# Performance work log

Hardware: AMD Instinct MI355X
Metric: run time of the kernel (lower is better)

Reference implementation:

```python
import jax, jax.numpy as jnp
import numpy as np

E = 32      # embed_dim
F = 64      # ff_dim
S = 256     # input_dim == seq_len (each feature is a token)
O = 8       # output_dim
B = 2048    # batch


def _layernorm(x, g, b, eps=1e-5):
    mu = jnp.mean(x, axis=-1, keepdims=True)
    var = jnp.mean((x - mu) ** 2, axis=-1, keepdims=True)
    return (x - mu) * jax.lax.rsqrt(var + eps) * g + b


def setup_inputs() -> dict:
    key = jax.random.key(0)
    ks = jax.random.split(key, 16)
    s = 0.02
    return {
        "x": jax.random.normal(ks[0], (B, S), dtype=jnp.float32),
        # token_embed: Linear(1, E) -> weight is effectively a vector [E]
        "w_tok": jax.random.normal(ks[1], (E,), dtype=jnp.float32) * s,
        "b_tok": jnp.zeros((E,), dtype=jnp.float32),
        "pos": jax.random.normal(ks[2], (1, S, E), dtype=jnp.float32) * s,
        "wq": jax.random.normal(ks[3], (E, E), dtype=jnp.float32) * s,
        "bq": jnp.zeros((E,), dtype=jnp.float32),
        "wk": jax.random.normal(ks[4], (E, E), dtype=jnp.float32) * s,
        "bk": jnp.zeros((E,), dtype=jnp.float32),
        "wv": jax.random.normal(ks[5], (E, E), dtype=jnp.float32) * s,
        "bv": jnp.zeros((E,), dtype=jnp.float32),
        "w1": jax.random.normal(ks[6], (E, F), dtype=jnp.float32) * s,
        "b1": jnp.zeros((F,), dtype=jnp.float32),
        "w2": jax.random.normal(ks[7], (F, E), dtype=jnp.float32) * s,
        "b2": jnp.zeros((E,), dtype=jnp.float32),
        "g1": jnp.ones((E,), dtype=jnp.float32),
        "be1": jnp.zeros((E,), dtype=jnp.float32),
        "g2": jnp.ones((E,), dtype=jnp.float32),
        "be2": jnp.zeros((E,), dtype=jnp.float32),
        "wo": jax.random.normal(ks[8], (E, O), dtype=jnp.float32) * s,
        "bo": jnp.zeros((O,), dtype=jnp.float32),
    }


def reference(x, w_tok, b_tok, pos, wq, bq, wk, bk, wv, bv,
              w1, b1, w2, b2, g1, be1, g2, be2, wo, bo):
    # tokens: each scalar feature -> E-dim embedding, plus learned positions
    tokens = x[..., None] * w_tok + b_tok + pos[:, : x.shape[1], :]  # [B,S,E]
    q = tokens @ wq + bq
    k = tokens @ wk + bk
    v = tokens @ wv + bv
    scale = jnp.float32(1.0 / np.sqrt(E))
    attn = jax.nn.softmax(jnp.einsum("bqe,bke->bqk", q, k) * scale, axis=-1)
    attended = jnp.einsum("bqk,bke->bqe", attn, v)
    tokens = _layernorm(tokens + attended, g1, be1)
    ffn = jax.nn.gelu(tokens @ w1 + b1, approximate=False) @ w2 + b2
    tokens = _layernorm(tokens + ffn, g2, be2)
    pooled = jnp.mean(tokens, axis=1)  # [B,E]
    return pooled @ wo + bo            # [B,O]
```

## Files before the change

### kernel.cpp

```cpp
#include <hip/hip_runtime.h>

#define BATCH 2048
#define SEQ   256
#define E     32
#define FF    64
#define OUTD  8
#define ROWP  40

typedef float f32x4 __attribute__((ext_vector_type(4)));
typedef __bf16 bf16x4 __attribute__((ext_vector_type(4)));
typedef __bf16 bf16x8 __attribute__((ext_vector_type(8)));
typedef unsigned short ushort8 __attribute__((ext_vector_type(8)));

union FragU { unsigned int w[4]; ushort8 u; bf16x8 b; };

__device__ __forceinline__ unsigned short f2bf(float f) {
    union { float f; unsigned u; } x; x.f = f;
    unsigned r = x.u + 0x7fffu + ((x.u >> 16) & 1u);
    return (unsigned short)(r >> 16);
}
__device__ __forceinline__ float bf2f(unsigned short s) {
    union { unsigned u; float f; } x; x.u = ((unsigned)s) << 16;
    return x.f;
}

__device__ __forceinline__ FragU xposeLDS(ushort* scr, int lg, int lr,
                                          f32x4 c0, f32x4 c1) {
    bf16x4 a, b;
#pragma unroll
    for (int r = 0; r < 4; ++r) { a[r] = (__bf16)c0[r]; b[r] = (__bf16)c1[r]; }
    *(bf16x4*)(scr + lr * 40 + 4 * lg)      = a;
    *(bf16x4*)(scr + lr * 40 + 16 + 4 * lg) = b;
    FragU f;
    f.u = *(const ushort8*)(scr + lr * 40 + 8 * lg);
    return f;
}

__device__ __forceinline__ float gelu_poly(float u) {
    const float t2 = u * u;
    float q = fmaf(t2, 2.3087053e-4f, -2.3746564e-3f);
    q = fmaf(t2, q, 1.9947114e-2f);
    q = fmaf(t2, q, -1.3298076e-1f);
    q = fmaf(t2, q, 7.9788456e-1f);
    return fmaf(0.5f * t2, q, 0.5f * u);
}

__global__ void prepack_kernel(const float* __restrict__ wq,
                               const float* __restrict__ wk,
                               const float* __restrict__ wv,
                               const float* __restrict__ w1,
                               const float* __restrict__ w2,
                               ushort* __restrict__ ws)
{
    for (int slot = threadIdx.x; slot < 14 * 64; slot += 256) {
        const int tile = slot >> 6, lane = slot & 63;
        const int lg = lane >> 4, lr = lane & 15;
        const float* W; int N, kt, nt;
        if (tile < 2)       { W = wq; N = 32; kt = 0;              nt = tile;          }
        else if (tile < 4)  { W = wk; N = 32; kt = 0;              nt = tile - 2;      }
        else if (tile < 6)  { W = wv; N = 32; kt = 0;              nt = tile - 4;      }
        else if (tile < 10) { W = w1; N = 64; kt = 0;              nt = tile - 6;      }
        else                { W = w2; N = 32; kt = (tile-10) >> 1; nt = (tile-10) & 1; }
        ushort8 u;
#pragma unroll
        for (int i = 0; i < 8; ++i)
            u[i] = f2bf(W[(kt * 32 + 8 * lg + i) * N + nt * 16 + lr]);
        *(ushort8*)(ws + slot * 8) = u;
    }
}

__global__ __launch_bounds__(512, 4) void attn_model_kernel(
    const float* __restrict__ x,
    const float* __restrict__ w_tok,
    const float* __restrict__ b_tok,
    const float* __restrict__ pos,
    const float* __restrict__ bq,
    const float* __restrict__ bk,
    const float* __restrict__ bv,
    const float* __restrict__ b1,
    const float* __restrict__ b2,
    const float* __restrict__ g1, const float* __restrict__ be1,
    const float* __restrict__ g2, const float* __restrict__ be2,
    const float* __restrict__ wo, const float* __restrict__ bo,
    const ushort* __restrict__ wsp,
    float* __restrict__ out)
{
    __shared__ __align__(16) unsigned char SMEM[53376];
    ushort* R1u = (ushort*)SMEM;
    ushort* R2u = (ushort*)(SMEM + 20480);
    float*  ps  = (float*)(SMEM + 51200);

    const int b    = blockIdx.x;
    const int t    = threadIdx.x;
    const int lane = t & 63;
    const int w    = t >> 6;
    const int lg   = lane >> 4;
    const int lr   = lane & 15;
    const int rowbase = 32 * w;
    ushort* scr = (ushort*)(SMEM + 40960 + w * 1280);

    float x_t = 0.f;
    if (t < SEQ) {
        x_t = x[b * SEQ + t];
#pragma unroll
        for (int c = 0; c < 4; ++c) {
            bf16x8 v;
#pragma unroll
            for (int i = 0; i < 8; ++i) {
                const int e = c * 8 + i;
                v[i] = (__bf16)fmaf(x_t, w_tok[e], b_tok[e] + pos[t * E + e]);
            }
            *(bf16x8*)(R1u + t * ROWP + c * 8) = v;
        }
    }
    __syncthreads();

    FragU ta[2];
#pragma unroll
    for (int mt = 0; mt < 2; ++mt)
        ta[mt].u = *(const ushort8*)(R1u + (rowbase + 16 * mt + lr) * ROWP + 8 * lg);
    __syncthreads();

    const float kq = 0.25503987869054154f;
    FragU qa[2];
    {
        FragU wf0, wf1;
        wf0.u = *(const ushort8*)(wsp + (0 * 64 + lane) * 8);
        wf1.u = *(const ushort8*)(wsp + (1 * 64 + lane) * 8);
        const f32x4 bi0 = *(const f32x4*)(bq + 4 * lg);
        const f32x4 bi1 = *(const f32x4*)(bq + 16 + 4 * lg);
#pragma unroll
        for (int mt = 0; mt < 2; ++mt) {
            f32x4 c0 = __builtin_amdgcn_mfma_f32_16x16x32_bf16(wf0.b, ta[mt].b, bi0, 0, 0, 0);
            f32x4 c1 = __builtin_amdgcn_mfma_f32_16x16x32_bf16(wf1.b, ta[mt].b, bi1, 0, 0, 0);
            c0 *= kq; c1 *= kq;
            qa[mt] = xposeLDS(scr, lg, lr, c0, c1);
        }
    }
    {
        FragU wf0, wf1;
        wf0.u = *(const ushort8*)(wsp + (2 * 64 + lane) * 8);
        wf1.u = *(const ushort8*)(wsp + (3 * 64 + lane) * 8);
        const f32x4 bi0 = *(const f32x4*)(bk + 4 * lg);
        const f32x4 bi1 = *(const f32x4*)(bk + 16 + 4 * lg);
#pragma unroll
        for (int mt = 0; mt < 2; ++mt) {
            f32x4 c0 = __builtin_amdgcn_mfma_f32_16x16x32_bf16(wf0.b, ta[mt].b, bi0, 0, 0, 0);
            f32x4 c1 = __builtin_amdgcn_mfma_f32_16x16x32_bf16(wf1.b, ta[mt].b, bi1, 0, 0, 0);
            FragU kfr = xposeLDS(scr, lg, lr, c0, c1);
            *(ushort8*)(R2u + ((2 * w + mt) * 64 + lane) * 8) = kfr.u;
        }
    }
    {
        FragU wf0, wf1;
        wf0.u = *(const ushort8*)(wsp + (4 * 64 + lane) * 8);
        wf1.u = *(const ushort8*)(wsp + (5 * 64 + lane) * 8);
        const float bv0 = bv[lr], bv1 = bv[16 + lr];
        const f32x4 ib0 = {bv0, bv0, bv0, bv0};
        const f32x4 ib1 = {bv1, bv1, bv1, bv1};
        {
            f32x4 cA = __builtin_amdgcn_mfma_f32_16x16x32_bf16(ta[0].b, wf0.b, ib0, 0, 0, 0);
            f32x4 cB = __builtin_amdgcn_mfma_f32_16x16x32_bf16(ta[1].b, wf0.b, ib0, 0, 0, 0);
            FragU vfr = xposeLDS(scr, lg, lr, cA, cB);
            *(ushort8*)(R1u + ((w) * 64 + lane) * 8) = vfr.u;
        }
        {
            f32x4 cA = __builtin_amdgcn_mfma_f32_16x16x32_bf16(ta[0].b, wf1.b, ib1, 0, 0, 0);
            f32x4 cB = __builtin_amdgcn_mfma_f32_16x16x32_bf16(ta[1].b, wf1.b, ib1, 0, 0, 0);
            FragU vfr = xposeLDS(scr, lg, lr, cA, cB);
            *(ushort8*)(R1u + ((8 + w) * 64 + lane) * 8) = vfr.u;
        }
    }
    __syncthreads();

    f32x4 ot[2][2];
#pragma unroll
    for (int qt = 0; qt < 2; ++qt)
#pragma unroll
        for (int nt = 0; nt < 2; ++nt) { ot[qt][nt][0]=0.f; ot[qt][nt][1]=0.f; ot[qt][nt][2]=0.f; ot[qt][nt][3]=0.f; }
    float lpart[2] = {0.f, 0.f};
    const f32x4 z4 = {0.f, 0.f, 0.f, 0.f};

    for (int cb = 0; cb < 8; ++cb) {
        FragU kf0, kf1, vf0, vf1;
        kf0.u = *(const ushort8*)(R2u + ((2 * cb    ) * 64 + lane) * 8);
        kf1.u = *(const ushort8*)(R2u + ((2 * cb + 1) * 64 + lane) * 8);
        vf0.u = *(const ushort8*)(R1u + ((cb        ) * 64 + lane) * 8);
        vf1.u = *(const ushort8*)(R1u + ((8 + cb    ) * 64 + lane) * 8);
#pragma unroll
        for (int qt = 0; qt < 2; ++qt) {
            f32x4 s0 = __builtin_amdgcn_mfma_f32_16x16x32_bf16(kf0.b, qa[qt].b, z4, 0, 0, 0);
            f32x4 s1 = __builtin_amdgcn_mfma_f32_16x16x32_bf16(kf1.b, qa[qt].b, z4, 0, 0, 0);
            f32x4 p0, p1;
#pragma unroll
            for (int r = 0; r < 4; ++r) p0[r] = __builtin_amdgcn_exp2f(s0[r]);
#pragma unroll
            for (int r = 0; r < 4; ++r) p1[r] = __builtin_amdgcn_exp2f(s1[r]);
            lpart[qt] += ((p0[0]+p0[1]) + (p0[2]+p0[3])) + ((p1[0]+p1[1]) + (p1[2]+p1[3]));
            FragU pf = xposeLDS(scr, lg, lr, p0, p1);
            ot[qt][0] = __builtin_amdgcn_mfma_f32_16x16x32_bf16(vf0.b, pf.b, ot[qt][0], 0, 0, 0);
            ot[qt][1] = __builtin_amdgcn_mfma_f32_16x16x32_bf16(vf1.b, pf.b, ot[qt][1], 0, 0, 0);
        }
    }

    float linv[2];
#pragma unroll
    for (int qt = 0; qt < 2; ++qt) {
        float s = lpart[qt];
        s += __shfl_xor(s, 16);
        s += __shfl_xor(s, 32);
        linv[qt] = 1.0f / s;
    }
    __syncthreads();

#pragma unroll
    for (int qt = 0; qt < 2; ++qt) {
        f32x4 n0 = ot[qt][0] * linv[qt];
        f32x4 n1 = ot[qt][1] * linv[qt];
        FragU af = xposeLDS(scr, lg, lr, n0, n1);
        *(ushort8*)(R2u + (rowbase + 16 * qt + lr) * ROWP + 8 * lg) = af.u;
    }
    __syncthreads();

    if (t < SEQ) {
        float h[E];
        FragU ar[4];
#pragma unroll
        for (int c = 0; c < 4; ++c)
            ar[c].u = *(const ushort8*)(R2u + t * ROWP + c * 8);
#pragma unroll
        for (int c = 0; c < 4; ++c)
#pragma unroll
            for (int i = 0; i < 8; ++i) {
                const int e = c * 8 + i;
                h[e] = fmaf(x_t, w_tok[e], b_tok[e] + pos[t * E + e]) + (float)ar[c].b[i];
            }
        float mu = 0.f;
#pragma unroll
        for (int e = 0; e < E; ++e) mu += h[e];
        mu *= (1.f / E);
        float var = 0.f;
#pragma unroll
        for (int e = 0; e < E; ++e) { const float d = h[e] - mu; var = fmaf(d, d, var); }
        var *= (1.f / E);
        const float rstd = rsqrtf(var + 1e-5f);
#pragma unroll
        for (int c = 0; c < 4; ++c) {
            bf16x8 v;
#pragma unroll
            for (int i = 0; i < 8; ++i) {
                const int e = c * 8 + i;
                v[i] = (__bf16)fmaf((h[e] - mu) * rstd, g1[e], be1[e]);
            }
            *(bf16x8*)(R1u + t * ROWP + c * 8) = v;
        }
    }
    __syncthreads();

    FragU ha[2];
#pragma unroll
    for (int mt = 0; mt < 2; ++mt)
        ha[mt].u = *(const ushort8*)(R1u + (rowbase + 16 * mt + lr) * ROWP + 8 * lg);

    f32x4 c2t[2][2];
    {
        const f32x4 ib20 = *(const f32x4*)(b2 + 4 * lg);
        const f32x4 ib21 = *(const f32x4*)(b2 + 16 + 4 * lg);
#pragma unroll
        for (int mt = 0; mt < 2; ++mt) { c2t[mt][0] = ib20; c2t[mt][1] = ib21; }
    }
#pragma unroll
    for (int hh = 0; hh < 2; ++hh) {
        FragU w1a, w1b, w2a, w2b;
        w1a.u = *(const ushort8*)(wsp + ((6 + 2 * hh) * 64 + lane) * 8);
        w1b.u = *(const ushort8*)(wsp + ((7 + 2 * hh) * 64 + lane) * 8);
        w2a.u = *(const ushort8*)(wsp + ((10 + 2 * hh) * 64 + lane) * 8);
        w2b.u = *(const ushort8*)(wsp + ((11 + 2 * hh) * 64 + lane) * 8);
        const f32x4 ib10 = *(const f32x4*)(b1 + 32 * hh + 4 * lg);
        const f32x4 ib11 = *(const f32x4*)(b1 + 32 * hh + 16 + 4 * lg);
#pragma unroll
        for (int mt = 0; mt < 2; ++mt) {
            f32x4 f0  = __builtin_amdgcn_mfma_f32_16x16x32_bf16(w1a.b, ha[mt].b, ib10, 0, 0, 0);
            f32x4 f1v = __builtin_amdgcn_mfma_f32_16x16x32_bf16(w1b.b, ha[mt].b, ib11, 0, 0, 0);
#pragma unroll
            for (int r = 0; r < 4; ++r) { f0[r] = gelu_poly(f0[r]); f1v[r] = gelu_poly(f1v[r]); }
            FragU faf = xposeLDS(scr, lg, lr, f0, f1v);
            c2t[mt][0] = __builtin_amdgcn_mfma_f32_16x16x32_bf16(w2a.b, faf.b, c2t[mt][0], 0, 0, 0);
            c2t[mt][1] = __builtin_amdgcn_mfma_f32_16x16x32_bf16(w2b.b, faf.b, c2t[mt][1], 0, 0, 0);
        }
    }
#pragma unroll
    for (int mt = 0; mt < 2; ++mt) {
        FragU ff = xposeLDS(scr, lg, lr, c2t[mt][0], c2t[mt][1]);
        *(ushort8*)(R2u + (rowbase + 16 * mt + lr) * ROWP + 8 * lg) = ff.u;
    }
    __syncthreads();

    if (t < SEQ) {
        float h2[E];
        FragU fr[4], hr[4];
#pragma unroll
        for (int c = 0; c < 4; ++c) {
            fr[c].u = *(const ushort8*)(R2u + t * ROWP + c * 8);
            hr[c].u = *(const ushort8*)(R1u + t * ROWP + c * 8);
        }
#pragma unroll
        for (int c = 0; c < 4; ++c)
#pragma unroll
            for (int i = 0; i < 8; ++i)
                h2[c * 8 + i] = (float)hr[c].b[i] + (float)fr[c].b[i];
        float mu = 0.f;
#pragma unroll
        for (int e = 0; e < E; ++e) mu += h2[e];
        mu *= (1.f / E);
        float var = 0.f;
#pragma unroll
        for (int e = 0; e < E; ++e) { const float d = h2[e] - mu; var = fmaf(d, d, var); }
        var *= (1.f / E);
        const float rstd = rsqrtf(var + 1e-5f);
#pragma unroll
        for (int c = 0; c < 4; ++c) {
            bf16x8 v;
#pragma unroll
            for (int i = 0; i < 8; ++i) {
                const int e = c * 8 + i;
                v[i] = (__bf16)fmaf((h2[e] - mu) * rstd, g2[e], be2[e]);
            }
            *(bf16x8*)(R1u + t * ROWP + c * 8) = v;
        }
    }
    __syncthreads();

    {
        const int e = t & 31;
        const int g = t >> 5;
        float psum = 0.f;
#pragma unroll 8
        for (int r = 0; r < 16; ++r)
            psum += bf2f(R1u[(g * 16 + r) * ROWP + e]);
        ps[g * 32 + e] = psum;
    }
    __syncthreads();

    if (t < E) {
        float s = 0.f;
#pragma unroll
        for (int g = 0; g < 16; ++g) s += ps[g * 32 + t];
        ps[512 + t] = s * (1.f / SEQ);
    }
    if (t < OUTD) {
        float acc = bo[t];
#pragma unroll
        for (int e = 0; e < E; ++e)
            acc = fmaf(ps[512 + e], wo[e * OUTD + t], acc);
        out[b * OUTD + t] = acc;
    }
}

extern "C" void kernel_launch(void* const* d_in, const int* in_sizes, int n_in,
                              void* d_out, int out_size, void* d_ws, size_t ws_size,
                              hipStream_t stream) {
    const float* x     = (const float*)d_in[0];
    const float* w_tok = (const float*)d_in[1];
    const float* b_tok = (const float*)d_in[2];
    const float* pos   = (const float*)d_in[3];
    const float* wq    = (const float*)d_in[4];
    const float* bq    = (const float*)d_in[5];
    const float* wk    = (const float*)d_in[6];
    const float* bk    = (const float*)d_in[7];
    const float* wv    = (const float*)d_in[8];
    const float* bv    = (const float*)d_in[9];
    const float* w1    = (const float*)d_in[10];
    const float* b1    = (const float*)d_in[11];
    const float* w2    = (const float*)d_in[12];
    const float* b2    = (const float*)d_in[13];
    const float* g1    = (const float*)d_in[14];
    const float* be1   = (const float*)d_in[15];
    const float* g2    = (const float*)d_in[16];
    const float* be2   = (const float*)d_in[17];
    const float* wo    = (const float*)d_in[18];
    const float* bo    = (const float*)d_in[19];
    float* outp        = (float*)d_out;
    ushort* wsp        = (ushort*)d_ws;

    prepack_kernel<<<dim3(1), dim3(256), 0, stream>>>(wq, wk, wv, w1, w2, wsp);
    attn_model_kernel<<<dim3(BATCH), dim3(512), 0, stream>>>(
        x, w_tok, b_tok, pos, bq, bk, bv, b1, b2,
        g1, be1, g2, be2, wo, bo, wsp, outp);
}
```

Baseline: 67.25 us.

## Build token fragments in registers and make layernorms wave-local across all threads

Token embedding fragments are now computed straight into MFMA operand registers instead of being staged through shared memory, which removes two block-wide barriers. Both layernorms are split over two threads per token, so all 512 threads take part instead of 256. Each wave now handles only the 32 rows it produced itself, which lets the barriers around the layernorms be dropped. The pooling scratch buffer is aliased onto the per-wave transpose area to shrink shared memory; in exchange, embedding loads from global memory are duplicated, and the extra lane shuffles add a dependency on wave-local LDS ordering.

```diff
diff --git a/kernel.cpp b/kernel.cpp
--- a/kernel.cpp
+++ b/kernel.cpp
@@ -22,6 +22,11 @@
 __device__ __forceinline__ float bf2f(unsigned short s) {
     union { unsigned u; float f; } x; x.u = ((unsigned)s) << 16;
     return x.f;
+}
+__device__ __forceinline__ unsigned packbf(float lo, float hi) {
+    union { __bf16 h[2]; unsigned u; } p;
+    p.h[0] = (__bf16)lo; p.h[1] = (__bf16)hi;
+    return p.u;
 }
 
 __device__ __forceinline__ FragU xposeLDS(ushort* scr, int lg, int lr,
@@ -85,10 +90,10 @@
     const ushort* __restrict__ wsp,
     float* __restrict__ out)
 {
-    __shared__ __align__(16) unsigned char SMEM[53376];
+    __shared__ __align__(16) unsigned char SMEM[51200];
     ushort* R1u = (ushort*)SMEM;
     ushort* R2u = (ushort*)(SMEM + 20480);
-    float*  ps  = (float*)(SMEM + 51200);
+    float*  ps  = (float*)(SMEM + 40960);
 
     const int b    = blockIdx.x;
     const int t    = threadIdx.x;
@@ -97,29 +102,25 @@
     const int lg   = lane >> 4;
     const int lr   = lane & 15;
     const int rowbase = 32 * w;
+    const int tokh = t >> 1;
+    const int hf   = t & 1;
     ushort* scr = (ushort*)(SMEM + 40960 + w * 1280);
 
-    float x_t = 0.f;
-    if (t < SEQ) {
-        x_t = x[b * SEQ + t];
-#pragma unroll
-        for (int c = 0; c < 4; ++c) {
-            bf16x8 v;
-#pragma unroll
-            for (int i = 0; i < 8; ++i) {
-                const int e = c * 8 + i;
-                v[i] = (__bf16)fmaf(x_t, w_tok[e], b_tok[e] + pos[t * E + e]);
-            }
-            *(bf16x8*)(R1u + t * ROWP + c * 8) = v;
-        }
-    }
-    __syncthreads();
-
     FragU ta[2];
 #pragma unroll
-    for (int mt = 0; mt < 2; ++mt)
-        ta[mt].u = *(const ushort8*)(R1u + (rowbase + 16 * mt + lr) * ROWP + 8 * lg);
-    __syncthreads();
+    for (int mt = 0; mt < 2; ++mt) {
+        const int row = rowbase + 16 * mt + lr;
+        const float xv = x[b * SEQ + row];
+        const float* pp = pos + row * E + 8 * lg;
+        const float* wt = w_tok + 8 * lg;
+        const float* bt = b_tok + 8 * lg;
+#pragma unroll
+        for (int j = 0; j < 4; ++j) {
+            const float v0 = fmaf(xv, wt[2 * j],     bt[2 * j]     + pp[2 * j]);
+            const float v1 = fmaf(xv, wt[2 * j + 1], bt[2 * j + 1] + pp[2 * j + 1]);
+            ta[mt].w[j] = packbf(v0, v1);
+        }
+    }
 
     const float kq = 0.25503987869054154f;
     FragU qa[2];
@@ -220,42 +221,42 @@
         FragU af = xposeLDS(scr, lg, lr, n0, n1);
         *(ushort8*)(R2u + (rowbase + 16 * qt + lr) * ROWP + 8 * lg) = af.u;
     }
-    __syncthreads();
-
-    if (t < SEQ) {
-        float h[E];
-        FragU ar[4];
-#pragma unroll
-        for (int c = 0; c < 4; ++c)
-            ar[c].u = *(const ushort8*)(R2u + t * ROWP + c * 8);
-#pragma unroll
-        for (int c = 0; c < 4; ++c)
+
+    {
+        float h[16];
+        FragU ar0, ar1;
+        ar0.u = *(const ushort8*)(R2u + tokh * ROWP + (2 * hf    ) * 8);
+        ar1.u = *(const ushort8*)(R2u + tokh * ROWP + (2 * hf + 1) * 8);
+        const float xv = x[b * SEQ + tokh];
+        const float* pp = pos + tokh * E + hf * 16;
+#pragma unroll
+        for (int i = 0; i < 16; ++i) {
+            const int e = hf * 16 + i;
+            const float att = (i < 8) ? (float)ar0.b[i] : (float)ar1.b[i - 8];
+            h[i] = fmaf(xv, w_tok[e], b_tok[e] + pp[i]) + att;
+        }
+        float s = 0.f;
+#pragma unroll
+        for (int i = 0; i < 16; ++i) s += h[i];
+        s += __shfl_xor(s, 1);
+        const float mu = s * (1.f / E);
+        float vs = 0.f;
+#pragma unroll
+        for (int i = 0; i < 16; ++i) { const float d = h[i] - mu; vs = fmaf(d, d, vs); }
+        vs += __shfl_xor(vs, 1);
+        const float rstd = rsqrtf(vs * (1.f / E) + 1e-5f);
+#pragma unroll
+        for (int cc = 0; cc < 2; ++cc) {
+            bf16x8 v;
 #pragma unroll
             for (int i = 0; i < 8; ++i) {
-                const int e = c * 8 + i;
-                h[e] = fmaf(x_t, w_tok[e], b_tok[e] + pos[t * E + e]) + (float)ar[c].b[i];
+                const int ii = cc * 8 + i;
+                const int e  = hf * 16 + ii;
+                v[i] = (__bf16)fmaf((h[ii] - mu) * rstd, g1[e], be1[e]);
             }
-        float mu = 0.f;
-#pragma unroll
-        for (int e = 0; e < E; ++e) mu += h[e];
-        mu *= (1.f / E);
-        float var = 0.f;
-#pragma unroll
-        for (int e = 0; e < E; ++e) { const float d = h[e] - mu; var = fmaf(d, d, var); }
-        var *= (1.f / E);
-        const float rstd = rsqrtf(var + 1e-5f);
-#pragma unroll
-        for (int c = 0; c < 4; ++c) {
-            bf16x8 v;
-#pragma unroll
-            for (int i = 0; i < 8; ++i) {
-                const int e = c * 8 + i;
-                v[i] = (__bf16)fmaf((h[e] - mu) * rstd, g1[e], be1[e]);
-            }
-            *(bf16x8*)(R1u + t * ROWP + c * 8) = v;
-        }
-    }
-    __syncthreads();
+            *(bf16x8*)(R1u + tokh * ROWP + (2 * hf + cc) * 8) = v;
+        }
+    }
 
     FragU ha[2];
 #pragma unroll
@@ -294,39 +295,40 @@
         FragU ff = xposeLDS(scr, lg, lr, c2t[mt][0], c2t[mt][1]);
         *(ushort8*)(R2u + (rowbase + 16 * mt + lr) * ROWP + 8 * lg) = ff.u;
     }
-    __syncthreads();
-
-    if (t < SEQ) {
-        float h2[E];
-        FragU fr[4], hr[4];
-#pragma unroll
-        for (int c = 0; c < 4; ++c) {
-            fr[c].u = *(const ushort8*)(R2u + t * ROWP + c * 8);
-            hr[c].u = *(const ushort8*)(R1u + t * ROWP + c * 8);
-        }
-#pragma unroll
-        for (int c = 0; c < 4; ++c)
-#pragma unroll
-            for (int i = 0; i < 8; ++i)
-                h2[c * 8 + i] = (float)hr[c].b[i] + (float)fr[c].b[i];
-        float mu = 0.f;
-#pragma unroll
-        for (int e = 0; e < E; ++e) mu += h2[e];
-        mu *= (1.f / E);
-        float var = 0.f;
-#pragma unroll
-        for (int e = 0; e < E; ++e) { const float d = h2[e] - mu; var = fmaf(d, d, var); }
-        var *= (1.f / E);
-        const float rstd = rsqrtf(var + 1e-5f);
-#pragma unroll
-        for (int c = 0; c < 4; ++c) {
+
+    {
+        float h2[16];
+        FragU fr0, fr1, hr0, hr1;
+        fr0.u = *(const ushort8*)(R2u + tokh * ROWP + (2 * hf    ) * 8);
+        fr1.u = *(const ushort8*)(R2u + tokh * ROWP + (2 * hf + 1) * 8);
+        hr0.u = *(const ushort8*)(R1u + tokh * ROWP + (2 * hf    ) * 8);
+        hr1.u = *(const ushort8*)(R1u + tokh * ROWP + (2 * hf + 1) * 8);
+#pragma unroll
+        for (int i = 0; i < 16; ++i) {
+            const float fv = (i < 8) ? (float)fr0.b[i] : (float)fr1.b[i - 8];
+            const float hv = (i < 8) ? (float)hr0.b[i] : (float)hr1.b[i - 8];
+            h2[i] = hv + fv;
+        }
+        float s = 0.f;
+#pragma unroll
+        for (int i = 0; i < 16; ++i) s += h2[i];
+        s += __shfl_xor(s, 1);
+        const float mu = s * (1.f / E);
+        float vs = 0.f;
+#pragma unroll
+        for (int i = 0; i < 16; ++i) { const float d = h2[i] - mu; vs = fmaf(d, d, vs); }
+        vs += __shfl_xor(vs, 1);
+        const float rstd = rsqrtf(vs * (1.f / E) + 1e-5f);
+#pragma unroll
+        for (int cc = 0; cc < 2; ++cc) {
             bf16x8 v;
 #pragma unroll
             for (int i = 0; i < 8; ++i) {
-                const int e = c * 8 + i;
-                v[i] = (__bf16)fmaf((h2[e] - mu) * rstd, g2[e], be2[e]);
+                const int ii = cc * 8 + i;
+                const int e  = hf * 16 + ii;
+                v[i] = (__bf16)fmaf((h2[ii] - mu) * rstd, g2[e], be2[e]);
             }
-            *(bf16x8*)(R1u + t * ROWP + c * 8) = v;
+            *(bf16x8*)(R1u + tokh * ROWP + (2 * hf + cc) * 8) = v;
         }
     }
     __syncthreads();
```

Measured after the change: 64.71 us. 3.8% less time.
